# Kernel tuning notes

Measured on AMD Instinct MI355X. Metric: run time of the kernel, lower is better.

The kernel has to match this reference:

```python
import jax, jax.numpy as jnp
import numpy as np

B, SQ, SK, D = 32, 2048, 2048, 64


def setup_inputs() -> dict:
    key = jax.random.key(0)
    kq, kk, km = jax.random.split(key, 3)
    q = jax.random.normal(kq, (B, SQ, D), dtype=jnp.float32)
    k = jax.random.normal(kk, (B, SK, D), dtype=jnp.float32)
    mask = jax.random.randint(km, (B, SQ, SK), 0, 2, dtype=jnp.int32)
    return {"q": q, "k": k, "mask": mask}


def reference(q, k, mask):
    # scores = q @ k^T / sqrt(D)  -> [B, SQ, SK]
    scale = 1.0 / np.sqrt(q.shape[-1]).astype(np.float32)
    scores = jnp.einsum('bqd,bkd->bqk', q, k) * scale
    scores = jnp.where(mask == 0, -jnp.inf, scores)
    return jax.nn.softmax(scores, axis=-1)
```

## Files before the change

kernel.cpp:

```cpp
#include <hip/hip_runtime.h>
#include <math.h>

constexpr int BB  = 32;
constexpr int SQL = 2048;
constexpr int SKL = 2048;
constexpr int DD  = 64;

using f32x4 = __attribute__((ext_vector_type(4))) float;
using bfrag = __attribute__((ext_vector_type(8))) short;
typedef unsigned long long u64;

static __device__ __forceinline__ unsigned short f2bf(float x) {
    unsigned u = __float_as_uint(x);
    u = u + 0x7FFFu + ((u >> 16) & 1u);
    return (unsigned short)(u >> 16);
}
static __device__ __forceinline__ float bf2f(unsigned short h) {
    return __uint_as_float((unsigned)h << 16);
}

static __device__ __forceinline__ void gld16(const void* g, void* l) {
    __builtin_amdgcn_global_load_lds(
        (const __attribute__((address_space(1))) void*)(size_t)g,
        (__attribute__((address_space(3))) void*)(unsigned)(size_t)l,
        16, 0, 0);
}

__global__ __launch_bounds__(256) void compress_mask(
    const int* __restrict__ m, unsigned char* __restrict__ bm)
{
    const int t = threadIdx.x;
    const size_t g0 = (size_t)blockIdx.x * 1024 + t;
    const int4* mp = (const int4*)m;
    int4 a0 = mp[(g0)       * 2], a1 = mp[(g0)       * 2 + 1];
    int4 b0 = mp[(g0 + 256) * 2], b1 = mp[(g0 + 256) * 2 + 1];
    int4 c0 = mp[(g0 + 512) * 2], c1 = mp[(g0 + 512) * 2 + 1];
    int4 d0 = mp[(g0 + 768) * 2], d1 = mp[(g0 + 768) * 2 + 1];
#define PACK8(v0, v1)                                                         \
    (unsigned char)((v0.x != 0 ? 1u : 0u)  | (v0.y != 0 ? 2u : 0u)   |        \
                    (v0.z != 0 ? 4u : 0u)  | (v0.w != 0 ? 8u : 0u)   |        \
                    (v1.x != 0 ? 16u : 0u) | (v1.y != 0 ? 32u : 0u)  |        \
                    (v1.z != 0 ? 64u : 0u) | (v1.w != 0 ? 128u : 0u))
    bm[g0]       = PACK8(a0, a1);
    bm[g0 + 256] = PACK8(b0, b1);
    bm[g0 + 512] = PACK8(c0, c1);
    bm[g0 + 768] = PACK8(d0, d1);
#undef PACK8
}

__global__ __launch_bounds__(256) void split_k_swz(
    const float* __restrict__ k, unsigned char* __restrict__ kswz)
{
    const int i0 = blockIdx.x * blockDim.x + threadIdx.x;
    const int g  = i0 & 7;
    const int c  = (i0 >> 3) & 2047;
    const int b  = i0 >> 14;
    const float* kp = k + ((size_t)(b * 2048 + c)) * DD + g * 8;
    bfrag h, lo;
    #pragma unroll
    for (int j = 0; j < 8; ++j) {
        const float x = kp[j];
        const unsigned short hh = f2bf(x);
        h[j]  = (short)hh;
        lo[j] = (short)f2bf(x - bf2f(hh));
    }
    const int sw = (c & 7) << 4;
    unsigned char* rec = kswz + ((size_t)(b * 2048 + c)) * 256;
    *(bfrag*)(rec + ((g * 16) ^ sw))       = h;
    *(bfrag*)(rec + 128 + ((g * 16) ^ sw)) = lo;
}

template<bool PRE>
__global__ __launch_bounds__(512, 2) void sdpa_v13(
    const float* __restrict__ q, const float* __restrict__ k,
    const int* __restrict__ mask, const unsigned char* __restrict__ bm,
    const unsigned char* __restrict__ kswz, float* __restrict__ out)
{
    __shared__ char pool[8 * 12288 + 1024];

    const int t   = threadIdx.x;
    const int l   = t & 63;
    const int w   = t >> 6;
    const int lr  = l & 15;
    const int lg  = l >> 4;
    const int bid = blockIdx.x;
    const int swz = (bid & 7) * 256 + (bid >> 3);
    const int b   = swz >> 6;
    const int r0  = (swz & 63) * 32;
    const int c0  = w * 256;
    const size_t row0 = (size_t)b * SQL + (size_t)(r0 + lr);
    const size_t row1 = row0 + 16;
    const int swk = (lr & 7) << 4;

    char* kseg = pool + w * 12288;
    const char*  ksrc = PRE ? (const char*)(kswz + ((size_t)b * SKL + c0) * 256) : nullptr;
    const float* kraw = PRE ? nullptr : k + (size_t)b * SKL * DD;
    const int*   mr0  = PRE ? nullptr : mask + row0 * SKL + c0 + lg * 4;
    const int*   mr1  = PRE ? nullptr : mask + row1 * SKL + c0 + lg * 4;

#define STAGE(T)                                                               \
    do {                                                                       \
        char* _kd = kseg + ((T) % 3) * 4096;                                   \
        if constexpr (PRE) {                                                   \
            const char* _ks = ksrc + (size_t)(T) * 4096;                       \
            gld16(_ks + l * 16,        _kd + l * 16);                          \
            gld16(_ks + 1024 + l * 16, _kd + 1024 + l * 16);                   \
            gld16(_ks + 2048 + l * 16, _kd + 2048 + l * 16);                   \
            gld16(_ks + 3072 + l * 16, _kd + 3072 + l * 16);                   \
        } else {                                                               \
            const float* _kc = kraw + (size_t)(c0 + (T) * 16 + lr) * DD;       \
            const f32x4 _a0 = *(const f32x4*)(_kc + lg * 8);                   \
            const f32x4 _a1 = *(const f32x4*)(_kc + lg * 8 + 4);               \
            const f32x4 _b0 = *(const f32x4*)(_kc + (lg + 4) * 8);             \
            const f32x4 _b1 = *(const f32x4*)(_kc + (lg + 4) * 8 + 4);         \
            bfrag _h, _o;                                                      \
            _Pragma("unroll")                                                  \
            for (int _j = 0; _j < 4; ++_j) {                                   \
                unsigned short _t2;                                            \
                _t2 = f2bf(_a0[_j]); _h[_j]   = (short)_t2;                    \
                _o[_j]   = (short)f2bf(_a0[_j] - bf2f(_t2));                   \
                _t2 = f2bf(_a1[_j]); _h[_j+4] = (short)_t2;                    \
                _o[_j+4] = (short)f2bf(_a1[_j] - bf2f(_t2));                   \
            }                                                                  \
            char* _rec = _kd + lr * 256;                                       \
            *(bfrag*)(_rec + ((lg * 16) ^ swk))       = _h;                    \
            *(bfrag*)(_rec + 128 + ((lg * 16) ^ swk)) = _o;                    \
            _Pragma("unroll")                                                  \
            for (int _j = 0; _j < 4; ++_j) {                                   \
                unsigned short _t2;                                            \
                _t2 = f2bf(_b0[_j]); _h[_j]   = (short)_t2;                    \
                _o[_j]   = (short)f2bf(_b0[_j] - bf2f(_t2));                   \
                _t2 = f2bf(_b1[_j]); _h[_j+4] = (short)_t2;                    \
                _o[_j+4] = (short)f2bf(_b1[_j] - bf2f(_t2));                   \
            }                                                                  \
            *(bfrag*)(_rec + (((lg + 4) * 16) ^ swk))       = _h;              \
            *(bfrag*)(_rec + 128 + (((lg + 4) * 16) ^ swk)) = _o;              \
        }                                                                      \
    } while (0)

    STAGE(0);

    constexpr float QS = 0.18033688011112042f;
    bfrag qh0a, ql0a, qh1a, ql1a;
    bfrag qh0b, ql0b, qh1b, ql1b;
#define LOADQ(ROW, H0, L0, H1, L1)                                             \
    do {                                                                       \
        const float* _qp = q + (ROW) * DD + lg * 8;                            \
        const f32x4 _x0 = *(const f32x4*)_qp;                                  \
        const f32x4 _x1 = *(const f32x4*)(_qp + 4);                            \
        const f32x4 _y0 = *(const f32x4*)(_qp + 32);                           \
        const f32x4 _y1 = *(const f32x4*)(_qp + 36);                           \
        _Pragma("unroll")                                                      \
        for (int _j = 0; _j < 4; ++_j) {                                       \
            float _a = _x0[_j] * QS, _c = _x1[_j] * QS;                        \
            float _d = _y0[_j] * QS, _e = _y1[_j] * QS;                        \
            unsigned short _h;                                                 \
            _h = f2bf(_a); H0[_j]   = (short)_h; L0[_j]   = (short)f2bf(_a - bf2f(_h)); \
            _h = f2bf(_c); H0[_j+4] = (short)_h; L0[_j+4] = (short)f2bf(_c - bf2f(_h)); \
            _h = f2bf(_d); H1[_j]   = (short)_h; L1[_j]   = (short)f2bf(_d - bf2f(_h)); \
            _h = f2bf(_e); H1[_j+4] = (short)_h; L1[_j+4] = (short)f2bf(_e - bf2f(_h)); \
        }                                                                      \
    } while (0)
    LOADQ(row0, qh0a, ql0a, qh1a, ql1a);
    LOADQ(row1, qh0b, ql0b, qh1b, ql1b);
#undef LOADQ

    u64 ma0 = 0, ma1 = 0, ma2 = 0, ma3 = 0;
    u64 mb0 = 0, mb1 = 0, mb2 = 0, mb3 = 0;
    if constexpr (PRE) {
        const ulonglong2* wpa = (const ulonglong2*)(bm + row0 * (SKL / 8) + w * 32);
        const ulonglong2* wpb = (const ulonglong2*)(bm + row1 * (SKL / 8) + w * 32);
        const ulonglong2 va0 = wpa[0], va1 = wpa[1];
        const ulonglong2 vb0 = wpb[0], vb1 = wpb[1];
        ma0 = va0.x; ma1 = va0.y; ma2 = va1.x; ma3 = va1.y;
        mb0 = vb0.x; mb1 = vb0.y; mb2 = vb1.x; mb3 = vb1.y;
    }

    STAGE(1);
    STAGE(2);

    unsigned sc[64];
    float psum0 = 0.f, psum1 = 0.f;

#define ITER(T, VMC, MA, MB)                                                   \
    do {                                                                       \
        if constexpr (PRE)                                                     \
            asm volatile("s_waitcnt vmcnt(" #VMC ")" ::: "memory");            \
        const char* _c = kseg + ((T) % 3) * 4096 + lr * 256;                   \
        const bfrag _kh0 = *(const bfrag*)(_c + ((lg * 16) ^ swk));            \
        const bfrag _kh1 = *(const bfrag*)(_c + (((lg + 4) * 16) ^ swk));      \
        const bfrag _kl0 = *(const bfrag*)(_c + 128 + ((lg * 16) ^ swk));      \
        const bfrag _kl1 = *(const bfrag*)(_c + 128 + (((lg + 4) * 16) ^ swk));\
        int4 _mva, _mvb;                                                       \
        if constexpr (!PRE) {                                                  \
            _mva = *(const int4*)(mr0 + (T) * 16);                             \
            _mvb = *(const int4*)(mr1 + (T) * 16);                             \
        }                                                                      \
        asm volatile("s_waitcnt lgkmcnt(0)" ::: "memory");                     \
        __builtin_amdgcn_sched_barrier(0);                                     \
        if constexpr ((T) + 3 < 16) STAGE((T) + 3);                            \
                                          \
        f32x4 _h = {0.f, 0.f, 0.f, 0.f};                                       \
        f32x4 _m = {0.f, 0.f, 0.f, 0.f};                                       \
        _h = __builtin_amdgcn_mfma_f32_16x16x32_bf16(_kh0, qh0a, _h, 0, 0, 0); \
        _m = __builtin_amdgcn_mfma_f32_16x16x32_bf16(_kh0, ql0a, _m, 0, 0, 0); \
        _h = __builtin_amdgcn_mfma_f32_16x16x32_bf16(_kh1, qh1a, _h, 0, 0, 0); \
        _m = __builtin_amdgcn_mfma_f32_16x16x32_bf16(_kl0, qh0a, _m, 0, 0, 0); \
        _m = __builtin_amdgcn_mfma_f32_16x16x32_bf16(_kh1, ql1a, _m, 0, 0, 0); \
        _m = __builtin_amdgcn_mfma_f32_16x16x32_bf16(_kl1, qh1a, _m, 0, 0, 0); \
        const f32x4 _s0 = _h + _m;                                             \
                                                                  \
        f32x4 _h2 = {0.f, 0.f, 0.f, 0.f};                                      \
        f32x4 _m2 = {0.f, 0.f, 0.f, 0.f};                                      \
        _h2 = __builtin_amdgcn_mfma_f32_16x16x32_bf16(_kh0, qh0b, _h2, 0, 0, 0);\
        _m2 = __builtin_amdgcn_mfma_f32_16x16x32_bf16(_kh0, ql0b, _m2, 0, 0, 0);\
        _h2 = __builtin_amdgcn_mfma_f32_16x16x32_bf16(_kh1, qh1b, _h2, 0, 0, 0);\
        _m2 = __builtin_amdgcn_mfma_f32_16x16x32_bf16(_kl0, qh0b, _m2, 0, 0, 0);\
        _m2 = __builtin_amdgcn_mfma_f32_16x16x32_bf16(_kh1, ql1b, _m2, 0, 0, 0);\
        _m2 = __builtin_amdgcn_mfma_f32_16x16x32_bf16(_kl1, qh1b, _m2, 0, 0, 0);\
        const f32x4 _s1 = _h2 + _m2;                                           \
        unsigned _n0, _n1;                                                     \
        if constexpr (PRE) {                                                   \
            _n0 = (unsigned)((MA) >> (((T) & 3) * 16 + lg * 4)) & 0xFu;        \
            _n1 = (unsigned)((MB) >> (((T) & 3) * 16 + lg * 4)) & 0xFu;        \
        } else {                                                               \
            _n0 = (_mva.x != 0 ? 1u : 0u) | (_mva.y != 0 ? 2u : 0u)            \
                | (_mva.z != 0 ? 4u : 0u) | (_mva.w != 0 ? 8u : 0u);           \
            _n1 = (_mvb.x != 0 ? 1u : 0u) | (_mvb.y != 0 ? 2u : 0u)            \
                | (_mvb.z != 0 ? 4u : 0u) | (_mvb.w != 0 ? 8u : 0u);           \
        }                                                                      \
        const float _e0 = (_n0 & 1u) ? exp2f(_s0[0]) : 0.f;                    \
        const float _e1 = (_n0 & 2u) ? exp2f(_s0[1]) : 0.f;                    \
        const float _e2 = (_n0 & 4u) ? exp2f(_s0[2]) : 0.f;                    \
        const float _e3 = (_n0 & 8u) ? exp2f(_s0[3]) : 0.f;                    \
        const float _f0 = (_n1 & 1u) ? exp2f(_s1[0]) : 0.f;                    \
        const float _f1 = (_n1 & 2u) ? exp2f(_s1[1]) : 0.f;                    \
        const float _f2 = (_n1 & 4u) ? exp2f(_s1[2]) : 0.f;                    \
        const float _f3 = (_n1 & 8u) ? exp2f(_s1[3]) : 0.f;                    \
        psum0 += (_e0 + _e1) + (_e2 + _e3);                                    \
        psum1 += (_f0 + _f1) + (_f2 + _f3);                                    \
        asm volatile("v_cvt_pk_bf16_f32 %0, %1, %2"                            \
                     : "=v"(sc[4 * (T)])     : "v"(_e0), "v"(_e1));            \
        asm volatile("v_cvt_pk_bf16_f32 %0, %1, %2"                            \
                     : "=v"(sc[4 * (T) + 1]) : "v"(_e2), "v"(_e3));            \
        asm volatile("v_cvt_pk_bf16_f32 %0, %1, %2"                            \
                     : "=v"(sc[4 * (T) + 2]) : "v"(_f0), "v"(_f1));            \
        asm volatile("v_cvt_pk_bf16_f32 %0, %1, %2"                            \
                     : "=v"(sc[4 * (T) + 3]) : "v"(_f2), "v"(_f3));            \
    } while (0)

    ITER(0,  8, ma0, mb0); ITER(1,  8, ma0, mb0);
    ITER(2,  8, ma0, mb0); ITER(3,  8, ma0, mb0);
    ITER(4,  8, ma1, mb1); ITER(5,  8, ma1, mb1);
    ITER(6,  8, ma1, mb1); ITER(7,  8, ma1, mb1);
    ITER(8,  8, ma2, mb2); ITER(9,  8, ma2, mb2);
    ITER(10, 8, ma2, mb2); ITER(11, 8, ma2, mb2);
    ITER(12, 8, ma3, mb3); ITER(13, 8, ma3, mb3);
    ITER(14, 4, ma3, mb3); ITER(15, 0, ma3, mb3);
#undef ITER
#undef STAGE

    psum0 += __shfl_xor(psum0, 16, 64);
    psum0 += __shfl_xor(psum0, 32, 64);
    psum1 += __shfl_xor(psum1, 16, 64);
    psum1 += __shfl_xor(psum1, 32, 64);

    float* s_red = (float*)(pool + 8 * 12288);
    __syncthreads();
    if (l < 16) {
        s_red[w * 32 + lr]      = psum0;
        s_red[w * 32 + 16 + lr] = psum1;
    }
    __syncthreads();

    float tot0 = 0.f, tot1 = 0.f;
    #pragma unroll
    for (int ww = 0; ww < 8; ++ww) {
        tot0 += s_red[ww * 32 + lr];
        tot1 += s_red[ww * 32 + 16 + lr];
    }
    const float rinv0 = 1.0f / tot0;
    const float rinv1 = 1.0f / tot1;

    float* op0 = out + row0 * SKL + c0 + lg * 4;
    float* op1 = out + row1 * SKL + c0 + lg * 4;
    #pragma unroll
    for (int T = 0; T < 16; ++T) {
        const unsigned pa = sc[4 * T], pb = sc[4 * T + 1];
        const unsigned pc = sc[4 * T + 2], pd = sc[4 * T + 3];
        f32x4 o0, o1;
        o0[0] = bf2f((unsigned short)(pa & 0xffffu)) * rinv0;
        o0[1] = bf2f((unsigned short)(pa >> 16))     * rinv0;
        o0[2] = bf2f((unsigned short)(pb & 0xffffu)) * rinv0;
        o0[3] = bf2f((unsigned short)(pb >> 16))     * rinv0;
        o1[0] = bf2f((unsigned short)(pc & 0xffffu)) * rinv1;
        o1[1] = bf2f((unsigned short)(pc >> 16))     * rinv1;
        o1[2] = bf2f((unsigned short)(pd & 0xffffu)) * rinv1;
        o1[3] = bf2f((unsigned short)(pd >> 16))     * rinv1;
        *reinterpret_cast<f32x4*>(op0 + T * 16) = o0;
        *reinterpret_cast<f32x4*>(op1 + T * 16) = o1;
    }
}

extern "C" void kernel_launch(void* const* d_in, const int* in_sizes, int n_in,
                              void* d_out, int out_size, void* d_ws, size_t ws_size,
                              hipStream_t stream) {
    const float* q    = (const float*)d_in[0];
    const float* k    = (const float*)d_in[1];
    const int*   mask = (const int*)d_in[2];
    float*       out  = (float*)d_out;

    const size_t BM_B = (size_t)BB * SQL * SKL / 8;
    const size_t KS_B = (size_t)BB * SKL * 256;

    dim3 grid(2048);

    if (ws_size >= BM_B + KS_B) {
        unsigned char* bmp = (unsigned char*)d_ws;
        unsigned char* ksp = (unsigned char*)d_ws + BM_B;
        compress_mask<<<16384, 256, 0, stream>>>(mask, bmp);
        split_k_swz<<<2048, 256, 0, stream>>>(k, ksp);
        sdpa_v13<true><<<grid, 512, 0, stream>>>(q, k, mask, bmp, ksp, out);
    } else {
        sdpa_v13<false><<<grid, 512, 0, stream>>>(q, k, mask, nullptr, nullptr, out);
    }
}
```

Before: 335.7 us.

## Drop mask compression pass; stream int32 mask in-kernel with rotating prefetch

Removes the separate compress_mask kernel, which read the full int32 mask and wrote a bitmask, and instead has the main attention kernel read the int32 mask directly. Mask loads are prefetched three tiles ahead in rotating registers alongside the K staging, and the vmcnt waits are retuned to match. This removes one full extra pass over the mask and a kernel launch, at the cost of more outstanding global loads and register pressure inside the main kernel.

```diff
diff --git a/kernel.cpp b/kernel.cpp
--- a/kernel.cpp
+++ b/kernel.cpp
@@ -24,28 +24,6 @@
         (const __attribute__((address_space(1))) void*)(size_t)g,
         (__attribute__((address_space(3))) void*)(unsigned)(size_t)l,
         16, 0, 0);
-}
-
-__global__ __launch_bounds__(256) void compress_mask(
-    const int* __restrict__ m, unsigned char* __restrict__ bm)
-{
-    const int t = threadIdx.x;
-    const size_t g0 = (size_t)blockIdx.x * 1024 + t;
-    const int4* mp = (const int4*)m;
-    int4 a0 = mp[(g0)       * 2], a1 = mp[(g0)       * 2 + 1];
-    int4 b0 = mp[(g0 + 256) * 2], b1 = mp[(g0 + 256) * 2 + 1];
-    int4 c0 = mp[(g0 + 512) * 2], c1 = mp[(g0 + 512) * 2 + 1];
-    int4 d0 = mp[(g0 + 768) * 2], d1 = mp[(g0 + 768) * 2 + 1];
-#define PACK8(v0, v1)                                                         \
-    (unsigned char)((v0.x != 0 ? 1u : 0u)  | (v0.y != 0 ? 2u : 0u)   |        \
-                    (v0.z != 0 ? 4u : 0u)  | (v0.w != 0 ? 8u : 0u)   |        \
-                    (v1.x != 0 ? 16u : 0u) | (v1.y != 0 ? 32u : 0u)  |        \
-                    (v1.z != 0 ? 64u : 0u) | (v1.w != 0 ? 128u : 0u))
-    bm[g0]       = PACK8(a0, a1);
-    bm[g0 + 256] = PACK8(b0, b1);
-    bm[g0 + 512] = PACK8(c0, c1);
-    bm[g0 + 768] = PACK8(d0, d1);
-#undef PACK8
 }
 
 __global__ __launch_bounds__(256) void split_k_swz(
@@ -70,11 +48,15 @@
     *(bfrag*)(rec + 128 + ((g * 16) ^ sw)) = lo;
 }
 
+#define MF(A, B, C) __builtin_amdgcn_mfma_f32_16x16x32_bf16((A), (B), (C), 0, 0, 0)
+#define NIB4(M) ((unsigned)((M).x ? 1u:0u) | ((M).y ? 2u:0u) |                 \
+                 ((M).z ? 4u:0u) | ((M).w ? 8u:0u))
+
 template<bool PRE>
-__global__ __launch_bounds__(512, 2) void sdpa_v13(
+__global__ __launch_bounds__(512, 2) void sdpa_v16(
     const float* __restrict__ q, const float* __restrict__ k,
-    const int* __restrict__ mask, const unsigned char* __restrict__ bm,
-    const unsigned char* __restrict__ kswz, float* __restrict__ out)
+    const int* __restrict__ mask, const unsigned char* __restrict__ kswz,
+    float* __restrict__ out)
 {
     __shared__ char pool[8 * 12288 + 1024];
 
@@ -95,8 +77,8 @@
     char* kseg = pool + w * 12288;
     const char*  ksrc = PRE ? (const char*)(kswz + ((size_t)b * SKL + c0) * 256) : nullptr;
     const float* kraw = PRE ? nullptr : k + (size_t)b * SKL * DD;
-    const int*   mr0  = PRE ? nullptr : mask + row0 * SKL + c0 + lg * 4;
-    const int*   mr1  = PRE ? nullptr : mask + row1 * SKL + c0 + lg * 4;
+    const int*   mr0  = mask + row0 * SKL + c0 + lg * 4;
+    const int*   mr1  = mask + row1 * SKL + c0 + lg * 4;
 
 #define STAGE(T)                                                               \
     do {                                                                       \
@@ -138,7 +120,13 @@
         }                                                                      \
     } while (0)
 
+    int4 mA0, mB0, mA1, mB1, mA2, mB2;
     STAGE(0);
+    mA0 = *(const int4*)(mr0);      mB0 = *(const int4*)(mr1);
+    STAGE(1);
+    mA1 = *(const int4*)(mr0 + 16); mB1 = *(const int4*)(mr1 + 16);
+    STAGE(2);
+    mA2 = *(const int4*)(mr0 + 32); mB2 = *(const int4*)(mr1 + 32);
 
     constexpr float QS = 0.18033688011112042f;
     bfrag qh0a, ql0a, qh1a, ql1a;
@@ -165,24 +153,10 @@
     LOADQ(row1, qh0b, ql0b, qh1b, ql1b);
 #undef LOADQ
 
-    u64 ma0 = 0, ma1 = 0, ma2 = 0, ma3 = 0;
-    u64 mb0 = 0, mb1 = 0, mb2 = 0, mb3 = 0;
-    if constexpr (PRE) {
-        const ulonglong2* wpa = (const ulonglong2*)(bm + row0 * (SKL / 8) + w * 32);
-        const ulonglong2* wpb = (const ulonglong2*)(bm + row1 * (SKL / 8) + w * 32);
-        const ulonglong2 va0 = wpa[0], va1 = wpa[1];
-        const ulonglong2 vb0 = wpb[0], vb1 = wpb[1];
-        ma0 = va0.x; ma1 = va0.y; ma2 = va1.x; ma3 = va1.y;
-        mb0 = vb0.x; mb1 = vb0.y; mb2 = vb1.x; mb3 = vb1.y;
-    }
-
-    STAGE(1);
-    STAGE(2);
-
     unsigned sc[64];
     float psum0 = 0.f, psum1 = 0.f;
 
-#define ITER(T, VMC, MA, MB)                                                   \
+#define ITER(T, VMC, MA, MB, DOPF)                                             \
     do {                                                                       \
         if constexpr (PRE)                                                     \
             asm volatile("s_waitcnt vmcnt(" #VMC ")" ::: "memory");            \
@@ -192,43 +166,38 @@
         const bfrag _kl0 = *(const bfrag*)(_c + 128 + ((lg * 16) ^ swk));      \
         const bfrag _kl1 = *(const bfrag*)(_c + 128 + (((lg + 4) * 16) ^ swk));\
         int4 _mva, _mvb;                                                       \
-        if constexpr (!PRE) {                                                  \
+        if constexpr (PRE) { _mva = MA; _mvb = MB; }                           \
+        else {                                                                 \
             _mva = *(const int4*)(mr0 + (T) * 16);                             \
             _mvb = *(const int4*)(mr1 + (T) * 16);                             \
         }                                                                      \
         asm volatile("s_waitcnt lgkmcnt(0)" ::: "memory");                     \
         __builtin_amdgcn_sched_barrier(0);                                     \
-        if constexpr ((T) + 3 < 16) STAGE((T) + 3);                            \
+        if constexpr ((T) + 3 < 16) {                                          \
+            STAGE((T) + 3);                                                    \
+            if constexpr (PRE) {                                               \
+                if (DOPF) {                                                    \
+                    MA = *(const int4*)(mr0 + ((T) + 3) * 16);                 \
+                    MB = *(const int4*)(mr1 + ((T) + 3) * 16);                 \
+                }                                                              \
+            }                                                                  \
+        }                                                                      \
                                           \
         f32x4 _h = {0.f, 0.f, 0.f, 0.f};                                       \
         f32x4 _m = {0.f, 0.f, 0.f, 0.f};                                       \
-        _h = __builtin_amdgcn_mfma_f32_16x16x32_bf16(_kh0, qh0a, _h, 0, 0, 0); \
-        _m = __builtin_amdgcn_mfma_f32_16x16x32_bf16(_kh0, ql0a, _m, 0, 0, 0); \
-        _h = __builtin_amdgcn_mfma_f32_16x16x32_bf16(_kh1, qh1a, _h, 0, 0, 0); \
-        _m = __builtin_amdgcn_mfma_f32_16x16x32_bf16(_kl0, qh0a, _m, 0, 0, 0); \
-        _m = __builtin_amdgcn_mfma_f32_16x16x32_bf16(_kh1, ql1a, _m, 0, 0, 0); \
-        _m = __builtin_amdgcn_mfma_f32_16x16x32_bf16(_kl1, qh1a, _m, 0, 0, 0); \
+        _h = MF(_kh0, qh0a, _h);  _m = MF(_kh0, ql0a, _m);                     \
+        _h = MF(_kh1, qh1a, _h);  _m = MF(_kl0, qh0a, _m);                     \
+        _m = MF(_kh1, ql1a, _m);  _m = MF(_kl1, qh1a, _m);                     \
         const f32x4 _s0 = _h + _m;                                             \
                                                                   \
         f32x4 _h2 = {0.f, 0.f, 0.f, 0.f};                                      \
         f32x4 _m2 = {0.f, 0.f, 0.f, 0.f};                                      \
-        _h2 = __builtin_amdgcn_mfma_f32_16x16x32_bf16(_kh0, qh0b, _h2, 0, 0, 0);\
-        _m2 = __builtin_amdgcn_mfma_f32_16x16x32_bf16(_kh0, ql0b, _m2, 0, 0, 0);\
-        _h2 = __builtin_amdgcn_mfma_f32_16x16x32_bf16(_kh1, qh1b, _h2, 0, 0, 0);\
-        _m2 = __builtin_amdgcn_mfma_f32_16x16x32_bf16(_kl0, qh0b, _m2, 0, 0, 0);\
-        _m2 = __builtin_amdgcn_mfma_f32_16x16x32_bf16(_kh1, ql1b, _m2, 0, 0, 0);\
-        _m2 = __builtin_amdgcn_mfma_f32_16x16x32_bf16(_kl1, qh1b, _m2, 0, 0, 0);\
+        _h2 = MF(_kh0, qh0b, _h2);  _m2 = MF(_kh0, ql0b, _m2);                 \
+        _h2 = MF(_kh1, qh1b, _h2);  _m2 = MF(_kl0, qh0b, _m2);                 \
+        _m2 = MF(_kh1, ql1b, _m2);  _m2 = MF(_kl1, qh1b, _m2);                 \
         const f32x4 _s1 = _h2 + _m2;                                           \
-        unsigned _n0, _n1;                                                     \
-        if constexpr (PRE) {                                                   \
-            _n0 = (unsigned)((MA) >> (((T) & 3) * 16 + lg * 4)) & 0xFu;        \
-            _n1 = (unsigned)((MB) >> (((T) & 3) * 16 + lg * 4)) & 0xFu;        \
-        } else {                                                               \
-            _n0 = (_mva.x != 0 ? 1u : 0u) | (_mva.y != 0 ? 2u : 0u)            \
-                | (_mva.z != 0 ? 4u : 0u) | (_mva.w != 0 ? 8u : 0u);           \
-            _n1 = (_mvb.x != 0 ? 1u : 0u) | (_mvb.y != 0 ? 2u : 0u)            \
-                | (_mvb.z != 0 ? 4u : 0u) | (_mvb.w != 0 ? 8u : 0u);           \
-        }                                                                      \
+        const unsigned _n0 = NIB4(_mva);                                       \
+        const unsigned _n1 = NIB4(_mvb);                                       \
         const float _e0 = (_n0 & 1u) ? exp2f(_s0[0]) : 0.f;                    \
         const float _e1 = (_n0 & 2u) ? exp2f(_s0[1]) : 0.f;                    \
         const float _e2 = (_n0 & 4u) ? exp2f(_s0[2]) : 0.f;                    \
@@ -249,14 +218,14 @@
                      : "=v"(sc[4 * (T) + 3]) : "v"(_f2), "v"(_f3));            \
     } while (0)
 
-    ITER(0,  8, ma0, mb0); ITER(1,  8, ma0, mb0);
-    ITER(2,  8, ma0, mb0); ITER(3,  8, ma0, mb0);
-    ITER(4,  8, ma1, mb1); ITER(5,  8, ma1, mb1);
-    ITER(6,  8, ma1, mb1); ITER(7,  8, ma1, mb1);
-    ITER(8,  8, ma2, mb2); ITER(9,  8, ma2, mb2);
-    ITER(10, 8, ma2, mb2); ITER(11, 8, ma2, mb2);
-    ITER(12, 8, ma3, mb3); ITER(13, 8, ma3, mb3);
-    ITER(14, 4, ma3, mb3); ITER(15, 0, ma3, mb3);
+    ITER(0,  12, mA0, mB0, 1); ITER(1,  12, mA1, mB1, 1);
+    ITER(2,  12, mA2, mB2, 1); ITER(3,  12, mA0, mB0, 1);
+    ITER(4,  12, mA1, mB1, 1); ITER(5,  12, mA2, mB2, 1);
+    ITER(6,  12, mA0, mB0, 1); ITER(7,  12, mA1, mB1, 1);
+    ITER(8,  12, mA2, mB2, 1); ITER(9,  12, mA0, mB0, 1);
+    ITER(10, 12, mA1, mB1, 1); ITER(11, 12, mA2, mB2, 1);
+    ITER(12, 12, mA0, mB0, 1); ITER(13, 12, mA1, mB1, 0);
+    ITER(14, 6,  mA2, mB2, 0); ITER(15, 0,  mA0, mB0, 0);
 #undef ITER
 #undef STAGE
 
@@ -310,18 +279,15 @@
     const int*   mask = (const int*)d_in[2];
     float*       out  = (float*)d_out;
 
-    const size_t BM_B = (size_t)BB * SQL * SKL / 8;
     const size_t KS_B = (size_t)BB * SKL * 256;
 
     dim3 grid(2048);
 
-    if (ws_size >= BM_B + KS_B) {
-        unsigned char* bmp = (unsigned char*)d_ws;
-        unsigned char* ksp = (unsigned char*)d_ws + BM_B;
-        compress_mask<<<16384, 256, 0, stream>>>(mask, bmp);
+    if (ws_size >= KS_B) {
+        unsigned char* ksp = (unsigned char*)d_ws;
         split_k_swz<<<2048, 256, 0, stream>>>(k, ksp);
-        sdpa_v13<true><<<grid, 512, 0, stream>>>(q, k, mask, bmp, ksp, out);
+        sdpa_v16<true><<<grid, 512, 0, stream>>>(q, k, mask, ksp, out);
     } else {
-        sdpa_v13<false><<<grid, 512, 0, stream>>>(q, k, mask, nullptr, nullptr, out);
-    }
-}
+        sdpa_v16<false><<<grid, 512, 0, stream>>>(q, k, mask, nullptr, out);
+    }
+}
```

Measured after the change: 310.4 us. 7.5% less time.

## Drop K low-part split, widen blocks to 16 waves, shrink LDS ring

Applied to the files above, without the earlier changes.

K is now stored and used as a single bf16 value instead of a hi/lo pair, so each tile needs 4 MFMAs per row group instead of 6, and the preprocessed K buffer is half the size. Blocks grow to 1024 threads (16 waves of 128 columns each) and use a 4-slot, 2KB-per-slot LDS ring per wave. The fallback path no longer stages K through LDS and instead converts it from global memory directly. Dropping the K low part reduces the precision of the scores, which can hurt accuracy on the exponentiated softmax.

```diff
diff --git a/kernel.cpp b/kernel.cpp
--- a/kernel.cpp
+++ b/kernel.cpp
@@ -48,7 +48,7 @@
 #undef PACK8
 }
 
-__global__ __launch_bounds__(256) void split_k_swz(
+__global__ __launch_bounds__(256) void split_k1(
     const float* __restrict__ k, unsigned char* __restrict__ kswz)
 {
     const int i0 = blockIdx.x * blockDim.x + threadIdx.x;
@@ -56,27 +56,26 @@
     const int c  = (i0 >> 3) & 2047;
     const int b  = i0 >> 14;
     const float* kp = k + ((size_t)(b * 2048 + c)) * DD + g * 8;
-    bfrag h, lo;
+    bfrag h;
     #pragma unroll
-    for (int j = 0; j < 8; ++j) {
-        const float x = kp[j];
-        const unsigned short hh = f2bf(x);
-        h[j]  = (short)hh;
-        lo[j] = (short)f2bf(x - bf2f(hh));
-    }
-    const int sw = (c & 7) << 4;
-    unsigned char* rec = kswz + ((size_t)(b * 2048 + c)) * 256;
-    *(bfrag*)(rec + ((g * 16) ^ sw))       = h;
-    *(bfrag*)(rec + 128 + ((g * 16) ^ sw)) = lo;
-}
+    for (int j = 0; j < 8; ++j)
+        h[j] = (short)f2bf(kp[j]);
+    unsigned char* rec = kswz + ((size_t)(b * 2048 + c)) * 128;
+    *(bfrag*)(rec + 16 * (g ^ (c & 7))) = h;
+}
+
+#define MF(A, B, C) __builtin_amdgcn_mfma_f32_16x16x32_bf16((A), (B), (C), 0, 0, 0)
+#define NIB4(M) ((unsigned)((M).x ? 1u:0u) | ((M).y ? 2u:0u) |                 \
+                 ((M).z ? 4u:0u) | ((M).w ? 8u:0u))
 
 template<bool PRE>
-__global__ __launch_bounds__(512, 2) void sdpa_v13(
+__global__ __launch_bounds__(1024, 4) void sdpa_v19(
     const float* __restrict__ q, const float* __restrict__ k,
     const int* __restrict__ mask, const unsigned char* __restrict__ bm,
     const unsigned char* __restrict__ kswz, float* __restrict__ out)
 {
-    __shared__ char pool[8 * 12288 + 1024];
+    __shared__ char  kring[16][4][2048];
+    __shared__ float s_red[16][2][16];
 
     const int t   = threadIdx.x;
     const int l   = t & 63;
@@ -87,58 +86,16 @@
     const int swz = (bid & 7) * 256 + (bid >> 3);
     const int b   = swz >> 6;
     const int r0  = (swz & 63) * 32;
-    const int c0  = w * 256;
+    const int c0  = w * 128;
     const size_t row0 = (size_t)b * SQL + (size_t)(r0 + lr);
     const size_t row1 = row0 + 16;
-    const int swk = (lr & 7) << 4;
-
-    char* kseg = pool + w * 12288;
-    const char*  ksrc = PRE ? (const char*)(kswz + ((size_t)b * SKL + c0) * 256) : nullptr;
-    const float* kraw = PRE ? nullptr : k + (size_t)b * SKL * DD;
-    const int*   mr0  = PRE ? nullptr : mask + row0 * SKL + c0 + lg * 4;
-    const int*   mr1  = PRE ? nullptr : mask + row1 * SKL + c0 + lg * 4;
-
-#define STAGE(T)                                                               \
-    do {                                                                       \
-        char* _kd = kseg + ((T) % 3) * 4096;                                   \
-        if constexpr (PRE) {                                                   \
-            const char* _ks = ksrc + (size_t)(T) * 4096;                       \
-            gld16(_ks + l * 16,        _kd + l * 16);                          \
-            gld16(_ks + 1024 + l * 16, _kd + 1024 + l * 16);                   \
-            gld16(_ks + 2048 + l * 16, _kd + 2048 + l * 16);                   \
-            gld16(_ks + 3072 + l * 16, _kd + 3072 + l * 16);                   \
-        } else {                                                               \
-            const float* _kc = kraw + (size_t)(c0 + (T) * 16 + lr) * DD;       \
-            const f32x4 _a0 = *(const f32x4*)(_kc + lg * 8);                   \
-            const f32x4 _a1 = *(const f32x4*)(_kc + lg * 8 + 4);               \
-            const f32x4 _b0 = *(const f32x4*)(_kc + (lg + 4) * 8);             \
-            const f32x4 _b1 = *(const f32x4*)(_kc + (lg + 4) * 8 + 4);         \
-            bfrag _h, _o;                                                      \
-            _Pragma("unroll")                                                  \
-            for (int _j = 0; _j < 4; ++_j) {                                   \
-                unsigned short _t2;                                            \
-                _t2 = f2bf(_a0[_j]); _h[_j]   = (short)_t2;                    \
-                _o[_j]   = (short)f2bf(_a0[_j] - bf2f(_t2));                   \
-                _t2 = f2bf(_a1[_j]); _h[_j+4] = (short)_t2;                    \
-                _o[_j+4] = (short)f2bf(_a1[_j] - bf2f(_t2));                   \
-            }                                                                  \
-            char* _rec = _kd + lr * 256;                                       \
-            *(bfrag*)(_rec + ((lg * 16) ^ swk))       = _h;                    \
-            *(bfrag*)(_rec + 128 + ((lg * 16) ^ swk)) = _o;                    \
-            _Pragma("unroll")                                                  \
-            for (int _j = 0; _j < 4; ++_j) {                                   \
-                unsigned short _t2;                                            \
-                _t2 = f2bf(_b0[_j]); _h[_j]   = (short)_t2;                    \
-                _o[_j]   = (short)f2bf(_b0[_j] - bf2f(_t2));                   \
-                _t2 = f2bf(_b1[_j]); _h[_j+4] = (short)_t2;                    \
-                _o[_j+4] = (short)f2bf(_b1[_j] - bf2f(_t2));                   \
-            }                                                                  \
-            *(bfrag*)(_rec + (((lg + 4) * 16) ^ swk))       = _h;              \
-            *(bfrag*)(_rec + 128 + (((lg + 4) * 16) ^ swk)) = _o;              \
-        }                                                                      \
-    } while (0)
-
-    STAGE(0);
+
+    u64 ba0 = 0, ba1 = 0, bb0 = 0, bb1 = 0;
+    if constexpr (PRE) {
+        const ulonglong2 va = *(const ulonglong2*)(bm + row0 * (SKL / 8) + w * 16);
+        const ulonglong2 vb = *(const ulonglong2*)(bm + row1 * (SKL / 8) + w * 16);
+        ba0 = va.x; ba1 = va.y; bb0 = vb.x; bb1 = vb.y;
+    }
 
     constexpr float QS = 0.18033688011112042f;
     bfrag qh0a, ql0a, qh1a, ql1a;
@@ -164,70 +121,78 @@
     LOADQ(row0, qh0a, ql0a, qh1a, ql1a);
     LOADQ(row1, qh0b, ql0b, qh1b, ql1b);
 #undef LOADQ
-
-    u64 ma0 = 0, ma1 = 0, ma2 = 0, ma3 = 0;
-    u64 mb0 = 0, mb1 = 0, mb2 = 0, mb3 = 0;
-    if constexpr (PRE) {
-        const ulonglong2* wpa = (const ulonglong2*)(bm + row0 * (SKL / 8) + w * 32);
-        const ulonglong2* wpb = (const ulonglong2*)(bm + row1 * (SKL / 8) + w * 32);
-        const ulonglong2 va0 = wpa[0], va1 = wpa[1];
-        const ulonglong2 vb0 = wpb[0], vb1 = wpb[1];
-        ma0 = va0.x; ma1 = va0.y; ma2 = va1.x; ma3 = va1.y;
-        mb0 = vb0.x; mb1 = vb0.y; mb2 = vb1.x; mb3 = vb1.y;
-    }
-
+    __builtin_amdgcn_sched_barrier(0);
+
+    const char*  ksrc = PRE ? (const char*)(kswz + ((size_t)b * SKL + c0) * 128) : nullptr;
+    const float* kraw = PRE ? nullptr : k + (size_t)b * SKL * DD;
+    const int*   mr0  = PRE ? nullptr : mask + row0 * SKL + c0 + lg * 4;
+    const int*   mr1  = PRE ? nullptr : mask + row1 * SKL + c0 + lg * 4;
+    char* kseg = &kring[w][0][0];
+
+#define STAGE(T)                                                               \
+    do {                                                                       \
+        if constexpr (PRE) {                                                   \
+            char* _kd = kseg + (((T) & 3) << 11);                              \
+            const char* _ks = ksrc + (size_t)(T) * 2048;                       \
+            gld16(_ks + l * 16,        _kd + l * 16);                          \
+            gld16(_ks + 1024 + l * 16, _kd + 1024 + l * 16);                   \
+        }                                                                      \
+    } while (0)
+
+    STAGE(0);
     STAGE(1);
     STAGE(2);
 
-    unsigned sc[64];
+    unsigned sc[32];
     float psum0 = 0.f, psum1 = 0.f;
 
-#define ITER(T, VMC, MA, MB)                                                   \
+#define ITER(T, VMC, MW0, MW1)                                                 \
     do {                                                                       \
-        if constexpr (PRE)                                                     \
+        bfrag _kh0, _kh1;                                                      \
+        int4 _mva, _mvb;                                                       \
+        if constexpr (PRE) {                                                   \
             asm volatile("s_waitcnt vmcnt(" #VMC ")" ::: "memory");            \
-        const char* _c = kseg + ((T) % 3) * 4096 + lr * 256;                   \
-        const bfrag _kh0 = *(const bfrag*)(_c + ((lg * 16) ^ swk));            \
-        const bfrag _kh1 = *(const bfrag*)(_c + (((lg + 4) * 16) ^ swk));      \
-        const bfrag _kl0 = *(const bfrag*)(_c + 128 + ((lg * 16) ^ swk));      \
-        const bfrag _kl1 = *(const bfrag*)(_c + 128 + (((lg + 4) * 16) ^ swk));\
-        int4 _mva, _mvb;                                                       \
-        if constexpr (!PRE) {                                                  \
+            const char* _c = kseg + (((T) & 3) << 11) + lr * 128;              \
+            _kh0 = *(const bfrag*)(_c + 16 * (lg ^ (lr & 7)));                 \
+            _kh1 = *(const bfrag*)(_c + 16 * ((4 | lg) ^ (lr & 7)));           \
+            asm volatile("s_waitcnt lgkmcnt(0)" ::: "memory");                 \
+            __builtin_amdgcn_sched_barrier(0);                                 \
+            if constexpr ((T) + 3 < 8) STAGE((T) + 3);                         \
+        } else {                                                               \
+            const float* _kc = kraw + (size_t)(c0 + (T) * 16 + lr) * DD;       \
+            const f32x4 _v0 = *(const f32x4*)(_kc + lg * 8);                   \
+            const f32x4 _v1 = *(const f32x4*)(_kc + lg * 8 + 4);               \
+            const f32x4 _v2 = *(const f32x4*)(_kc + 32 + lg * 8);              \
+            const f32x4 _v3 = *(const f32x4*)(_kc + 36 + lg * 8);              \
+            _Pragma("unroll")                                                  \
+            for (int _j = 0; _j < 4; ++_j) {                                   \
+                _kh0[_j]     = (short)f2bf(_v0[_j]);                           \
+                _kh0[_j + 4] = (short)f2bf(_v1[_j]);                           \
+                _kh1[_j]     = (short)f2bf(_v2[_j]);                           \
+                _kh1[_j + 4] = (short)f2bf(_v3[_j]);                           \
+            }                                                                  \
             _mva = *(const int4*)(mr0 + (T) * 16);                             \
             _mvb = *(const int4*)(mr1 + (T) * 16);                             \
         }                                                                      \
-        asm volatile("s_waitcnt lgkmcnt(0)" ::: "memory");                     \
-        __builtin_amdgcn_sched_barrier(0);                                     \
-        if constexpr ((T) + 3 < 16) STAGE((T) + 3);                            \
-                                          \
+                              \
         f32x4 _h = {0.f, 0.f, 0.f, 0.f};                                       \
         f32x4 _m = {0.f, 0.f, 0.f, 0.f};                                       \
-        _h = __builtin_amdgcn_mfma_f32_16x16x32_bf16(_kh0, qh0a, _h, 0, 0, 0); \
-        _m = __builtin_amdgcn_mfma_f32_16x16x32_bf16(_kh0, ql0a, _m, 0, 0, 0); \
-        _h = __builtin_amdgcn_mfma_f32_16x16x32_bf16(_kh1, qh1a, _h, 0, 0, 0); \
-        _m = __builtin_amdgcn_mfma_f32_16x16x32_bf16(_kl0, qh0a, _m, 0, 0, 0); \
-        _m = __builtin_amdgcn_mfma_f32_16x16x32_bf16(_kh1, ql1a, _m, 0, 0, 0); \
-        _m = __builtin_amdgcn_mfma_f32_16x16x32_bf16(_kl1, qh1a, _m, 0, 0, 0); \
+        _h = MF(_kh0, qh0a, _h);  _m = MF(_kh0, ql0a, _m);                     \
+        _h = MF(_kh1, qh1a, _h);  _m = MF(_kh1, ql1a, _m);                     \
         const f32x4 _s0 = _h + _m;                                             \
                                                                   \
         f32x4 _h2 = {0.f, 0.f, 0.f, 0.f};                                      \
         f32x4 _m2 = {0.f, 0.f, 0.f, 0.f};                                      \
-        _h2 = __builtin_amdgcn_mfma_f32_16x16x32_bf16(_kh0, qh0b, _h2, 0, 0, 0);\
-        _m2 = __builtin_amdgcn_mfma_f32_16x16x32_bf16(_kh0, ql0b, _m2, 0, 0, 0);\
-        _h2 = __builtin_amdgcn_mfma_f32_16x16x32_bf16(_kh1, qh1b, _h2, 0, 0, 0);\
-        _m2 = __builtin_amdgcn_mfma_f32_16x16x32_bf16(_kl0, qh0b, _m2, 0, 0, 0);\
-        _m2 = __builtin_amdgcn_mfma_f32_16x16x32_bf16(_kh1, ql1b, _m2, 0, 0, 0);\
-        _m2 = __builtin_amdgcn_mfma_f32_16x16x32_bf16(_kl1, qh1b, _m2, 0, 0, 0);\
+        _h2 = MF(_kh0, qh0b, _h2);  _m2 = MF(_kh0, ql0b, _m2);                 \
+        _h2 = MF(_kh1, qh1b, _h2);  _m2 = MF(_kh1, ql1b, _m2);                 \
         const f32x4 _s1 = _h2 + _m2;                                           \
         unsigned _n0, _n1;                                                     \
         if constexpr (PRE) {                                                   \
-            _n0 = (unsigned)((MA) >> (((T) & 3) * 16 + lg * 4)) & 0xFu;        \
-            _n1 = (unsigned)((MB) >> (((T) & 3) * 16 + lg * 4)) & 0xFu;        \
+            _n0 = (unsigned)((MW0) >> (((T) & 3) * 16 + lg * 4)) & 0xFu;       \
+            _n1 = (unsigned)((MW1) >> (((T) & 3) * 16 + lg * 4)) & 0xFu;       \
         } else {                                                               \
-            _n0 = (_mva.x != 0 ? 1u : 0u) | (_mva.y != 0 ? 2u : 0u)            \
-                | (_mva.z != 0 ? 4u : 0u) | (_mva.w != 0 ? 8u : 0u);           \
-            _n1 = (_mvb.x != 0 ? 1u : 0u) | (_mvb.y != 0 ? 2u : 0u)            \
-                | (_mvb.z != 0 ? 4u : 0u) | (_mvb.w != 0 ? 8u : 0u);           \
+            _n0 = NIB4(_mva);                                                  \
+            _n1 = NIB4(_mvb);                                                  \
         }                                                                      \
         const float _e0 = (_n0 & 1u) ? exp2f(_s0[0]) : 0.f;                    \
         const float _e1 = (_n0 & 2u) ? exp2f(_s0[1]) : 0.f;                    \
@@ -249,14 +214,10 @@
                      : "=v"(sc[4 * (T) + 3]) : "v"(_f2), "v"(_f3));            \
     } while (0)
 
-    ITER(0,  8, ma0, mb0); ITER(1,  8, ma0, mb0);
-    ITER(2,  8, ma0, mb0); ITER(3,  8, ma0, mb0);
-    ITER(4,  8, ma1, mb1); ITER(5,  8, ma1, mb1);
-    ITER(6,  8, ma1, mb1); ITER(7,  8, ma1, mb1);
-    ITER(8,  8, ma2, mb2); ITER(9,  8, ma2, mb2);
-    ITER(10, 8, ma2, mb2); ITER(11, 8, ma2, mb2);
-    ITER(12, 8, ma3, mb3); ITER(13, 8, ma3, mb3);
-    ITER(14, 4, ma3, mb3); ITER(15, 0, ma3, mb3);
+    ITER(0, 4, ba0, bb0); ITER(1, 4, ba0, bb0);
+    ITER(2, 4, ba0, bb0); ITER(3, 4, ba0, bb0);
+    ITER(4, 4, ba1, bb1); ITER(5, 4, ba1, bb1);
+    ITER(6, 2, ba1, bb1); ITER(7, 0, ba1, bb1);
 #undef ITER
 #undef STAGE
 
@@ -265,19 +226,17 @@
     psum1 += __shfl_xor(psum1, 16, 64);
     psum1 += __shfl_xor(psum1, 32, 64);
 
-    float* s_red = (float*)(pool + 8 * 12288);
-    __syncthreads();
     if (l < 16) {
-        s_red[w * 32 + lr]      = psum0;
-        s_red[w * 32 + 16 + lr] = psum1;
+        s_red[w][0][lr] = psum0;
+        s_red[w][1][lr] = psum1;
     }
     __syncthreads();
 
     float tot0 = 0.f, tot1 = 0.f;
     #pragma unroll
-    for (int ww = 0; ww < 8; ++ww) {
-        tot0 += s_red[ww * 32 + lr];
-        tot1 += s_red[ww * 32 + 16 + lr];
+    for (int ww = 0; ww < 16; ++ww) {
+        tot0 += s_red[ww][0][lr];
+        tot1 += s_red[ww][1][lr];
     }
     const float rinv0 = 1.0f / tot0;
     const float rinv1 = 1.0f / tot1;
@@ -285,7 +244,7 @@
     float* op0 = out + row0 * SKL + c0 + lg * 4;
     float* op1 = out + row1 * SKL + c0 + lg * 4;
     #pragma unroll
-    for (int T = 0; T < 16; ++T) {
+    for (int T = 0; T < 8; ++T) {
         const unsigned pa = sc[4 * T], pb = sc[4 * T + 1];
         const unsigned pc = sc[4 * T + 2], pd = sc[4 * T + 3];
         f32x4 o0, o1;
@@ -311,7 +270,7 @@
     float*       out  = (float*)d_out;
 
     const size_t BM_B = (size_t)BB * SQL * SKL / 8;
-    const size_t KS_B = (size_t)BB * SKL * 256;
+    const size_t KS_B = (size_t)BB * SKL * 128;
 
     dim3 grid(2048);
 
@@ -319,9 +278,9 @@
         unsigned char* bmp = (unsigned char*)d_ws;
         unsigned char* ksp = (unsigned char*)d_ws + BM_B;
         compress_mask<<<16384, 256, 0, stream>>>(mask, bmp);
-        split_k_swz<<<2048, 256, 0, stream>>>(k, ksp);
-        sdpa_v13<true><<<grid, 512, 0, stream>>>(q, k, mask, bmp, ksp, out);
+        split_k1<<<2048, 256, 0, stream>>>(k, ksp);
+        sdpa_v19<true><<<grid, 1024, 0, stream>>>(q, k, mask, bmp, ksp, out);
     } else {
-        sdpa_v13<false><<<grid, 512, 0, stream>>>(q, k, mask, nullptr, nullptr, out);
-    }
-}
+        sdpa_v19<false><<<grid, 1024, 0, stream>>>(q, k, mask, nullptr, nullptr, out);
+    }
+}
```

New measurement: 333.2 us. No clear change (-0.8%).
